# Kernel tuning notes

Measured on AMD Instinct MI355X. Metric: run time of the kernel, lower is better.

## Reference

```python
import jax, jax.numpy as jnp
import numpy as np

B, NQ, NK, D = 8, 2048, 2048, 256


def setup_inputs() -> dict:
    key = jax.random.key(0)
    ks = jax.random.split(key, 4)
    scale = 1.0 / np.sqrt(D)
    return {
        "query": jax.random.normal(ks[0], (B, NQ, D), dtype=jnp.float32),
        "key": jax.random.normal(ks[1], (B, NK, D), dtype=jnp.float32),
        "Wq": jax.random.normal(ks[2], (D, D), dtype=jnp.float32) * scale,
        "bq": jnp.zeros((D,), dtype=jnp.float32),
        "Wk": jax.random.normal(ks[3], (D, D), dtype=jnp.float32) * scale,
        "bk": jnp.zeros((D,), dtype=jnp.float32),
    }


def reference(query, key, Wq, bq, Wk, bk):
    # value = key (pre-projection), as in the torch module
    value = key
    # FFT over the sequence axis (dim=1), keep real part
    q = jnp.real(jnp.fft.fft(query, axis=1)).astype(query.dtype)
    # torch nn.Linear: y = x @ W.T + b
    q = q @ Wq.T + bq                      # [B, NQ, D]
    k = key @ Wk.T + bk                    # [B, NK, D]
    scale = 1.0 / jnp.sqrt(jnp.asarray(q.shape[-1], q.dtype))
    scores = jnp.einsum('bqd,bkd->bqk', q, k) * scale   # [B, NQ, NK]
    probs = jax.nn.softmax(scores, axis=-1)
    out = jnp.einsum('bqk,bkd->bqd', probs, value)       # [B, NQ, D]
    return out
```

## Files before the change

### kernel.cpp

```cpp
#include <hip/hip_runtime.h>

#define B_ 8
#define NQ_ 2048
#define NK_ 2048
#define D_ 256
#define KF_ 1056

typedef __attribute__((ext_vector_type(8))) short bf16x8_t;
typedef __attribute__((ext_vector_type(4))) float f32x4_t;

static __device__ __forceinline__ unsigned short f2bf(float x) {
  unsigned int u = __float_as_uint(x);
  unsigned int r = (u + 0x7FFFu + ((u >> 16) & 1u)) >> 16;
  return (unsigned short)r;
}
static __device__ __forceinline__ float bf2f(unsigned short b) {
  return __uint_as_float(((unsigned int)b) << 16);
}

typedef __attribute__((address_space(1))) unsigned int gas_u32;
typedef __attribute__((address_space(3))) unsigned int las_u32;
static __device__ __forceinline__ void gl16(const void* g, void* l) {
  __builtin_amdgcn_global_load_lds((const gas_u32*)g, (las_u32*)l, 16, 0, 0);
}

__global__ __launch_bounds__(256) void wsplit_kernel(const float* __restrict__ Wq,
                                                     const float* __restrict__ Wk,
                                                     unsigned short* __restrict__ Wqh,
                                                     unsigned short* __restrict__ Wql,
                                                     unsigned short* __restrict__ Wkh,
                                                     unsigned short* __restrict__ Wkl) {
  const int i = blockIdx.x * 256 + threadIdx.x;
  const int n = D_ * D_;
  const float* x = (i < n) ? Wq : Wk;
  unsigned short* xh = (i < n) ? Wqh : Wkh;
  unsigned short* xl = (i < n) ? Wql : Wkl;
  const int j = (i < n) ? i : i - n;
  const float v = x[j];
  const unsigned short hb = f2bf(v);
  xh[j] = hb;
  xl[j] = f2bf(v - bf2f(hb));
}

__global__ __launch_bounds__(256) void key_split_vt(const float* __restrict__ key,
                                                    unsigned short* __restrict__ keyh,
                                                    unsigned short* __restrict__ keyl,
                                                    unsigned short* __restrict__ Vt) {
  __shared__ unsigned short lds[32][258];
  const int t = threadIdx.x;
  const int j0 = blockIdx.x * 32;
  const int b  = blockIdx.y;
#pragma unroll
  for (int p = 0; p < 32; ++p) {
    const size_t g = ((size_t)b * NK_ + j0 + p) * D_ + t;
    const float v = key[g];
    const unsigned short hb = f2bf(v);
    keyh[g] = hb;
    keyl[g] = f2bf(v - bf2f(hb));
    lds[p][t] = hb;
  }
  __syncthreads();
#pragma unroll
  for (int p = 0; p < 32; ++p) {
    const int jj = t & 31;
    const int d  = (t >> 5) + 8 * p;
    Vt[((size_t)b * D_ + d) * NK_ + j0 + jj] = lds[jj][d];
  }
}

__global__ __launch_bounds__(256) void cos_split_kernel(unsigned short* __restrict__ Ch,
                                                        unsigned short* __restrict__ Cl) {
  const int idx = blockIdx.x * 256 + threadIdx.x;
  const int i = idx / KF_, n = idx % KF_;
  float c = 0.f;
  if (n <= 1024) {
    const int m = (i * n) & 2047;
    c = cosf((float)m * 0.0030679615757712823f);
  }
  const unsigned short hb = f2bf(c);
  Ch[idx] = hb;
  Cl[idx] = f2bf(c - bf2f(hb));
}

__global__ __launch_bounds__(256) void qtf_split_kernel(const float* __restrict__ q,
                                                        unsigned short* __restrict__ Qtfh,
                                                        unsigned short* __restrict__ Qtfl) {
  __shared__ float lds[32][33];
  const int t  = threadIdx.x;
  const int n0 = blockIdx.x * 32;
  const int d0 = blockIdx.y * 32;
  const int b  = blockIdx.z;
#pragma unroll
  for (int p = 0; p < 4; ++p) {
    const int idx = t + 256 * p;
    const int dd = idx & 31, nn = idx >> 5;
    const int n = n0 + nn;
    float v = 0.f;
    if (n <= 1024) v = q[((size_t)b * NQ_ + n) * D_ + d0 + dd];
    if (n >= 1 && n <= 1023) v += q[((size_t)b * NQ_ + (2048 - n)) * D_ + d0 + dd];
    lds[nn][dd] = v;
  }
  __syncthreads();
#pragma unroll
  for (int p = 0; p < 4; ++p) {
    const int idx = t + 256 * p;
    const int nn = idx & 31, dd = idx >> 5;
    const float v = lds[nn][dd];
    const unsigned short hb = f2bf(v);
    const size_t o = ((size_t)b * D_ + d0 + dd) * KF_ + n0 + nn;
    Qtfh[o] = hb;
    Qtfl[o] = f2bf(v - bf2f(hb));
  }
}

__global__ __launch_bounds__(256, 2) void dft_mfma(const unsigned short* __restrict__ Ch,
                                                   const unsigned short* __restrict__ Cl,
                                                   const unsigned short* __restrict__ Qtfh,
                                                   const unsigned short* __restrict__ Qtfl,
                                                   float* __restrict__ qr) {
  __shared__ __align__(16) unsigned short Ah[128][40];
  __shared__ __align__(16) unsigned short Al[128][40];
  __shared__ __align__(16) unsigned short Bh[128][40];
  __shared__ __align__(16) unsigned short Bl[128][40];
  const int t = threadIdx.x;
  const int b = blockIdx.z / 3, split = blockIdx.z % 3;
  const int i0 = blockIdx.x * 128, d0 = blockIdx.y * 128;
  const int w = t >> 6, lane = t & 63, quad = lane >> 4, l16 = lane & 15;
  const int wq = w & 1, wj = w >> 1;
  float* qrs = qr + (size_t)split * ((size_t)B_ * 1152 * D_);

  f32x4_t acc[4][4];
#pragma unroll
  for (int a = 0; a < 4; ++a)
#pragma unroll
    for (int c = 0; c < 4; ++c) acc[a][c] = (f32x4_t)0.f;

  const size_t abase = (size_t)i0 * KF_;
  const size_t bbase = ((size_t)b * D_ + d0) * KF_;

  for (int c0 = split * 352; c0 < split * 352 + 352; c0 += 32) {
#pragma unroll
    for (int it = 0; it < 2; ++it) {
      const int unit = t + 256 * it;
      const int row = unit >> 2, u = (unit & 3) * 8;
      const size_t go = (size_t)row * KF_ + c0 + u;
      *(uint4*)&Ah[row][u] = *(const uint4*)&Ch[abase + go];
      *(uint4*)&Al[row][u] = *(const uint4*)&Cl[abase + go];
      *(uint4*)&Bh[row][u] = *(const uint4*)&Qtfh[bbase + go];
      *(uint4*)&Bl[row][u] = *(const uint4*)&Qtfl[bbase + go];
    }
    __syncthreads();
    {
      const int dcol = quad * 8;
      bf16x8_t ah[4], al[4], bh[4], bl[4];
#pragma unroll
      for (int x = 0; x < 4; ++x) {
        ah[x] = *(const bf16x8_t*)&Ah[wq * 64 + x * 16 + l16][dcol];
        al[x] = *(const bf16x8_t*)&Al[wq * 64 + x * 16 + l16][dcol];
        bh[x] = *(const bf16x8_t*)&Bh[wj * 64 + x * 16 + l16][dcol];
        bl[x] = *(const bf16x8_t*)&Bl[wj * 64 + x * 16 + l16][dcol];
      }
#pragma unroll
      for (int at = 0; at < 4; ++at)
#pragma unroll
        for (int jt = 0; jt < 4; ++jt) {
          acc[at][jt] = __builtin_amdgcn_mfma_f32_16x16x32_bf16(ah[at], bh[jt], acc[at][jt], 0, 0, 0);
          acc[at][jt] = __builtin_amdgcn_mfma_f32_16x16x32_bf16(ah[at], bl[jt], acc[at][jt], 0, 0, 0);
          acc[at][jt] = __builtin_amdgcn_mfma_f32_16x16x32_bf16(al[at], bh[jt], acc[at][jt], 0, 0, 0);
        }
    }
    __syncthreads();
  }
#pragma unroll
  for (int at = 0; at < 4; ++at) {
#pragma unroll
    for (int jt = 0; jt < 4; ++jt) {
      const int d = d0 + wj * 64 + jt * 16 + l16;
#pragma unroll
      for (int r = 0; r < 4; ++r) {
        const int i = i0 + wq * 64 + at * 16 + quad * 4 + r;
        qrs[((size_t)b * 1152 + i) * D_ + d] = acc[at][jt][r];
      }
    }
  }
}

__global__ __launch_bounds__(256) void qr_finalize_kernel(const float* __restrict__ qr,
                                                          unsigned short* __restrict__ qrh,
                                                          unsigned short* __restrict__ qrl) {
  const int i = blockIdx.x, b = blockIdx.y, d = threadIdx.x;
  const int src = (i <= 1087) ? i : (2048 - i);
  const size_t S = (size_t)B_ * 1152 * D_;
  const size_t idx = ((size_t)b * 1152 + src) * D_ + d;
  const float v = qr[idx] + qr[idx + S] + qr[idx + 2 * S];
  const unsigned short hb = f2bf(v);
  const size_t o = ((size_t)b * NQ_ + i) * D_ + d;
  qrh[o] = hb;
  qrl[o] = f2bf(v - bf2f(hb));
}

__global__ __launch_bounds__(256, 2) void proj_mfma2(
    const unsigned short* __restrict__ xh0, const unsigned short* __restrict__ xl0,
    const unsigned short* __restrict__ Wh0, const unsigned short* __restrict__ Wl0,
    const float* __restrict__ b0,
    unsigned short* __restrict__ yh0, unsigned short* __restrict__ yl0,
    const unsigned short* __restrict__ xh1, const unsigned short* __restrict__ xl1,
    const unsigned short* __restrict__ Wh1, const unsigned short* __restrict__ Wl1,
    const float* __restrict__ b1,
    unsigned short* __restrict__ yh1, unsigned short* __restrict__ yl1) {
  const int z = blockIdx.z;
  const unsigned short* xh = z ? xh1 : xh0;
  const unsigned short* xl = z ? xl1 : xl0;
  const unsigned short* Wh = z ? Wh1 : Wh0;
  const unsigned short* Wl = z ? Wl1 : Wl0;
  const float* bias = z ? b1 : b0;
  unsigned short* yh = z ? yh1 : yh0;
  unsigned short* yl = z ? yl1 : yl0;

  __shared__ __align__(16) unsigned short Xh[128][72];
  __shared__ __align__(16) unsigned short Xl[128][72];
  __shared__ __align__(16) unsigned short Bh[128][72];
  __shared__ __align__(16) unsigned short Bl[128][72];
  const int t = threadIdx.x;
  const int m0 = blockIdx.x * 128, o0 = blockIdx.y * 128;
  const int w = t >> 6, lane = t & 63, quad = lane >> 4, l16 = lane & 15;
  const int wq = w & 1, wj = w >> 1;

  f32x4_t acc[4][4];
#pragma unroll
  for (int a = 0; a < 4; ++a)
#pragma unroll
    for (int c = 0; c < 4; ++c) acc[a][c] = (f32x4_t)0.f;

  const size_t xbase = (size_t)m0 * D_;
  const size_t wbase = (size_t)o0 * D_;

  for (int c0 = 0; c0 < D_; c0 += 64) {
#pragma unroll
    for (int it = 0; it < 4; ++it) {
      const int unit = t + 256 * it;
      const int row = unit >> 3, u = (unit & 7) * 8;
      const size_t go = (size_t)row * D_ + c0 + u;
      *(uint4*)&Xh[row][u] = *(const uint4*)&xh[xbase + go];
      *(uint4*)&Xl[row][u] = *(const uint4*)&xl[xbase + go];
      *(uint4*)&Bh[row][u] = *(const uint4*)&Wh[wbase + go];
      *(uint4*)&Bl[row][u] = *(const uint4*)&Wl[wbase + go];
    }
    __syncthreads();
#pragma unroll
    for (int ks = 0; ks < 2; ++ks) {
      const int dcol = ks * 32 + quad * 8;
      bf16x8_t ah[4], al[4], bh[4], bl[4];
#pragma unroll
      for (int x = 0; x < 4; ++x) {
        ah[x] = *(const bf16x8_t*)&Xh[wq * 64 + x * 16 + l16][dcol];
        al[x] = *(const bf16x8_t*)&Xl[wq * 64 + x * 16 + l16][dcol];
        bh[x] = *(const bf16x8_t*)&Bh[wj * 64 + x * 16 + l16][dcol];
        bl[x] = *(const bf16x8_t*)&Bl[wj * 64 + x * 16 + l16][dcol];
      }
#pragma unroll
      for (int at = 0; at < 4; ++at)
#pragma unroll
        for (int jt = 0; jt < 4; ++jt) {
          acc[at][jt] = __builtin_amdgcn_mfma_f32_16x16x32_bf16(ah[at], bh[jt], acc[at][jt], 0, 0, 0);
          acc[at][jt] = __builtin_amdgcn_mfma_f32_16x16x32_bf16(ah[at], bl[jt], acc[at][jt], 0, 0, 0);
          acc[at][jt] = __builtin_amdgcn_mfma_f32_16x16x32_bf16(al[at], bh[jt], acc[at][jt], 0, 0, 0);
        }
    }
    __syncthreads();
  }
#pragma unroll
  for (int at = 0; at < 4; ++at) {
#pragma unroll
    for (int jt = 0; jt < 4; ++jt) {
      const int o = o0 + wj * 64 + jt * 16 + l16;
      const float bv = bias[o];
#pragma unroll
      for (int r = 0; r < 4; ++r) {
        const int m = m0 + wq * 64 + at * 16 + quad * 4 + r;
        const float v = acc[at][jt][r] + bv;
        const unsigned short hb = f2bf(v);
        yh[(size_t)m * D_ + o] = hb;
        yl[(size_t)m * D_ + o] = f2bf(v - bf2f(hb));
      }
    }
  }
}

__global__ __launch_bounds__(512, 4) void scores_p(const unsigned short* __restrict__ qh,
                                                   const unsigned short* __restrict__ ql,
                                                   const unsigned short* __restrict__ kh,
                                                   const unsigned short* __restrict__ kl,
                                                   unsigned short* __restrict__ Pb,
                                                   float2* __restrict__ stat) {
  __shared__ __align__(16) unsigned short Qh[128][64];
  __shared__ __align__(16) unsigned short Ql[128][64];
  __shared__ __align__(16) unsigned short Kh[128][64];
  __shared__ __align__(16) unsigned short Kl[128][64];
  __shared__ float mred[2][128];
  __shared__ float lred[2][128];
  const int t = threadIdx.x;
  const int b = blockIdx.z;
  const int i0 = blockIdx.x * 128, j0 = blockIdx.y * 128;
  const int jb = blockIdx.y;
  const int w = t >> 6, lane = t & 63, quad = lane >> 4, l16 = lane & 15;
  const int wq = w & 3, wj = w >> 2;
  const int sr0 = t >> 3, ssl = t & 7;

  f32x4_t acc[2][4];
#pragma unroll
  for (int x = 0; x < 2; ++x)
#pragma unroll
    for (int y = 0; y < 4; ++y) acc[x][y] = (f32x4_t)0.f;

  const size_t qbase = ((size_t)b * NQ_ + i0) * D_;
  const size_t kbase = ((size_t)b * NK_ + j0) * D_;

  auto STAGE = [&](int c0) {
#pragma unroll
    for (int half = 0; half < 2; ++half) {
      const int row = half * 64 + sr0;
      const int sg = (ssl ^ (row & 7)) * 8;
      const size_t ro = (size_t)row * D_ + c0 + sg;
      gl16(qh + qbase + ro, &Qh[half * 64 + w * 8][0]);
      gl16(ql + qbase + ro, &Ql[half * 64 + w * 8][0]);
      gl16(kh + kbase + ro, &Kh[half * 64 + w * 8][0]);
      gl16(kl + kbase + ro, &Kl[half * 64 + w * 8][0]);
    }
  };

  STAGE(0);

#pragma unroll
  for (int s = 0; s < 4; ++s) {
    asm volatile("s_waitcnt vmcnt(0)" ::: "memory");
    __builtin_amdgcn_s_barrier();
    asm volatile("" ::: "memory");

#pragma unroll
    for (int ks = 0; ks < 2; ++ks) {
      bf16x8_t ah[2], al[2], bh[4], bl[4];
#pragma unroll
      for (int x = 0; x < 2; ++x) {
        const int ar = wq * 32 + x * 16 + l16;
        const int asl = ((ks * 4 + quad) ^ (ar & 7)) * 8;
        ah[x] = *(const bf16x8_t*)&Qh[ar][asl];
        al[x] = *(const bf16x8_t*)&Ql[ar][asl];
      }
#pragma unroll
      for (int y = 0; y < 4; ++y) {
        const int br = wj * 64 + y * 16 + l16;
        const int bsl = ((ks * 4 + quad) ^ (br & 7)) * 8;
        bh[y] = *(const bf16x8_t*)&Kh[br][bsl];
        bl[y] = *(const bf16x8_t*)&Kl[br][bsl];
      }
#pragma unroll
      for (int x = 0; x < 2; ++x)
#pragma unroll
        for (int y = 0; y < 4; ++y) {
          acc[x][y] = __builtin_amdgcn_mfma_f32_16x16x32_bf16(ah[x], bh[y], acc[x][y], 0, 0, 0);
          acc[x][y] = __builtin_amdgcn_mfma_f32_16x16x32_bf16(ah[x], bl[y], acc[x][y], 0, 0, 0);
          acc[x][y] = __builtin_amdgcn_mfma_f32_16x16x32_bf16(al[x], bh[y], acc[x][y], 0, 0, 0);
        }
    }

    asm volatile("" ::: "memory");
    __builtin_amdgcn_s_barrier();
    asm volatile("" ::: "memory");
    if (s < 3) STAGE((s + 1) * 64);
  }

  const float scale = 0.0625f;
  float mt[2][4];
#pragma unroll
  for (int x = 0; x < 2; ++x)
#pragma unroll
    for (int r = 0; r < 4; ++r) mt[x][r] = -3e38f;
#pragma unroll
  for (int x = 0; x < 2; ++x)
#pragma unroll
    for (int y = 0; y < 4; ++y)
#pragma unroll
      for (int r = 0; r < 4; ++r) {
        acc[x][y][r] *= scale;
        mt[x][r] = fmaxf(mt[x][r], acc[x][y][r]);
      }
#pragma unroll
  for (int off = 1; off < 16; off <<= 1)
#pragma unroll
    for (int x = 0; x < 2; ++x)
#pragma unroll
      for (int r = 0; r < 4; ++r) mt[x][r] = fmaxf(mt[x][r], __shfl_xor(mt[x][r], off));
  if (l16 == 0) {
#pragma unroll
    for (int x = 0; x < 2; ++x)
#pragma unroll
      for (int r = 0; r < 4; ++r)
        mred[wj][wq * 32 + x * 16 + quad * 4 + r] = mt[x][r];
  }
  __syncthreads();
  float nrow[2][4], mu[2][4], lt[2][4];
#pragma unroll
  for (int x = 0; x < 2; ++x)
#pragma unroll
    for (int r = 0; r < 4; ++r) {
      const int rr = wq * 32 + x * 16 + quad * 4 + r;
      const float m = fmaxf(mred[0][rr], mred[1][rr]);
      const float n = ceilf(m * 1.44269504f);
      nrow[x][r] = n;
      mu[x][r] = n * 0.69314718056f;
      lt[x][r] = 0.f;
    }
  const size_t pbase = ((size_t)(b * 16 + jb)) * NQ_ * 128;
#pragma unroll
  for (int x = 0; x < 2; ++x)
#pragma unroll
    for (int y = 0; y < 4; ++y) {
      const int jloc = wj * 64 + y * 16 + l16;
#pragma unroll
      for (int r = 0; r < 4; ++r) {
        const int i = i0 + wq * 32 + x * 16 + quad * 4 + r;
        float p = __expf(acc[x][y][r] - mu[x][r]);
        p = fmaxf(p, 8.673617e-19f);
        lt[x][r] += p;
        Pb[pbase + (size_t)i * 128 + jloc] = f2bf(p);
      }
    }
#pragma unroll
  for (int off = 1; off < 16; off <<= 1)
#pragma unroll
    for (int x = 0; x < 2; ++x)
#pragma unroll
      for (int r = 0; r < 4; ++r) lt[x][r] += __shfl_xor(lt[x][r], off);
  if (l16 == 0) {
#pragma unroll
    for (int x = 0; x < 2; ++x)
#pragma unroll
      for (int r = 0; r < 4; ++r)
        lred[wj][wq * 32 + x * 16 + quad * 4 + r] = lt[x][r];
  }
  __syncthreads();
  if (wj == 0 && l16 == 0) {
#pragma unroll
    for (int x = 0; x < 2; ++x)
#pragma unroll
      for (int r = 0; r < 4; ++r) {
        const int rr = wq * 32 + x * 16 + quad * 4 + r;
        stat[(size_t)jb * (B_ * NQ_) + (size_t)b * NQ_ + i0 + rr] =
            make_float2(nrow[x][r], lred[0][rr] + lred[1][rr]);
      }
  }
}

__global__ __launch_bounds__(256) void rowfin_kernel(const float2* __restrict__ stat,
                                                     float2* __restrict__ srow) {
  const int i = blockIdx.x * 256 + threadIdx.x;
  float2 st[16];
  float m = -3e38f;
#pragma unroll
  for (int jb = 0; jb < 16; ++jb) {
    st[jb] = stat[(size_t)jb * (B_ * NQ_) + i];
    m = fmaxf(m, st[jb].x);
  }
  float l = 0.f;
#pragma unroll
  for (int jb = 0; jb < 16; ++jb) l += st[jb].y * exp2f(st[jb].x - m);
  srow[i] = make_float2(m, 1.0f / l);
}

__global__ __launch_bounds__(512, 1) void pv_p(const unsigned short* __restrict__ Pb,
                                               const float2* __restrict__ stat,
                                               const float2* __restrict__ srow,
                                               const unsigned short* __restrict__ Vt,
                                               float* __restrict__ out) {
  __shared__ __align__(16) unsigned short Ps[3][64][64];
  __shared__ __align__(16) unsigned short Vs[3][256][64];
  const int t = threadIdx.x;
  const int lb = (blockIdx.x & 7) * 32 + (blockIdx.x >> 3);
  const int mb = lb * 64;
  const int b  = lb >> 5;
  const int i0 = mb & (NQ_ - 1);
  const int w = t >> 6, lane = t & 63, quad = lane >> 4, l16 = lane & 15;
  const int wm = w & 1, wd = w >> 1;
  const int prow = t >> 3, pslot = t & 7;

  unsigned int es2[16][2];
  {
    float nmax[2];
#pragma unroll
    for (int x = 0; x < 2; ++x)
      nmax[x] = srow[mb + wm * 32 + x * 16 + l16].x;
#pragma unroll
    for (int jb = 0; jb < 16; ++jb)
#pragma unroll
      for (int x = 0; x < 2; ++x) {
        const int arow = mb + wm * 32 + x * 16 + l16;
        int e = (int)(nmax[x] - stat[(size_t)jb * (B_ * NQ_) + arow].x);
        e = e < 0 ? 0 : (e > 60 ? 60 : e);
        es2[jb][x] = (unsigned int)(e << 7) * 0x00010001u;
      }
  }

  f32x4_t acc[2][4];
#pragma unroll
  for (int x = 0; x < 2; ++x)
#pragma unroll
    for (int y = 0; y < 4; ++y) acc[x][y] = (f32x4_t)0.f;

  const size_t vbase = (size_t)b * D_ * (size_t)NK_;

  auto STAGE = [&](int nb, int s) {
    const int jj = s * 64;
    const int jb = jj >> 7, off = jj & 127;
    {
      const int sg = pslot ^ (prow & 7);
      gl16(Pb + ((size_t)(b * 16 + jb)) * NQ_ * 128 +
               (size_t)(i0 + prow) * 128 + off + sg * 8,
           &Ps[nb][w * 8][0]);
    }
#pragma unroll
    for (int k = 0; k < 4; ++k) {
      const int vrow = k * 64 + prow;
      const int sg = pslot ^ (vrow & 7);
      gl16(Vt + vbase + (size_t)vrow * NK_ + jj + sg * 8,
           &Vs[nb][k * 64 + w * 8][0]);
    }
  };

  asm volatile("s_waitcnt vmcnt(0)" ::: "memory");
  STAGE(0, 0);
  STAGE(1, 1);

#pragma unroll
  for (int s = 0; s < 32; ++s) {
    const int cb = s % 3;
    if (s < 30) {
      STAGE((s + 2) % 3, s + 2);
      asm volatile("s_waitcnt vmcnt(10)" ::: "memory");
    } else if (s == 30) {
      asm volatile("s_waitcnt vmcnt(5)" ::: "memory");
    } else {
      asm volatile("s_waitcnt vmcnt(0)" ::: "memory");
    }
    __builtin_amdgcn_s_barrier();
    asm volatile("" ::: "memory");

    const unsigned int e0 = es2[s >> 1][0], e1 = es2[s >> 1][1];
#pragma unroll
    for (int ks = 0; ks < 2; ++ks) {
      bf16x8_t a[2], bv[4];
#pragma unroll
      for (int x = 0; x < 2; ++x) {
        const int row = wm * 32 + x * 16 + l16;
        const int sk = (ks * 4 + quad) ^ (row & 7);
        uint4 u = *(const uint4*)&Ps[cb][row][sk * 8];
        const unsigned int e = (x == 0) ? e0 : e1;
        u.x -= e; u.y -= e; u.z -= e; u.w -= e;
        a[x] = *(const bf16x8_t*)&u;
      }
#pragma unroll
      for (int y = 0; y < 4; ++y) {
        const int row = wd * 64 + y * 16 + l16;
        const int sk = (ks * 4 + quad) ^ (row & 7);
        bv[y] = *(const bf16x8_t*)&Vs[cb][row][sk * 8];
      }
#pragma unroll
      for (int x = 0; x < 2; ++x)
#pragma unroll
        for (int y = 0; y < 4; ++y)
          acc[x][y] = __builtin_amdgcn_mfma_f32_16x16x32_bf16(a[x], bv[y], acc[x][y], 0, 0, 0);
    }

    asm volatile("" ::: "memory");
    __builtin_amdgcn_s_barrier();
    asm volatile("" ::: "memory");
  }

#pragma unroll
  for (int x = 0; x < 2; ++x) {
    float sy[4];
#pragma unroll
    for (int r = 0; r < 4; ++r)
      sy[r] = srow[mb + wm * 32 + x * 16 + quad * 4 + r].y;
#pragma unroll
    for (int y = 0; y < 4; ++y) {
      const int d = wd * 64 + y * 16 + l16;
#pragma unroll
      for (int r = 0; r < 4; ++r) {
        const int m = mb + wm * 32 + x * 16 + quad * 4 + r;
        out[(size_t)m * D_ + d] = acc[x][y][r] * sy[r];
      }
    }
  }
}

extern "C" void kernel_launch(void* const* d_in, const int* in_sizes, int n_in,
                              void* d_out, int out_size, void* d_ws, size_t ws_size,
                              hipStream_t stream) {
  const float* query = (const float*)d_in[0];
  const float* key   = (const float*)d_in[1];
  const float* Wq    = (const float*)d_in[2];
  const float* bq    = (const float*)d_in[3];
  const float* Wk    = (const float*)d_in[4];
  const float* bk    = (const float*)d_in[5];
  float* out = (float*)d_out;

  char* ws = (char*)d_ws;
  const size_t MB = (size_t)1 << 20;
  unsigned short* qh = (unsigned short*)(ws);
  unsigned short* ql = (unsigned short*)(ws + 8 * MB);
  unsigned short* kh = (unsigned short*)(ws + 16 * MB);
  unsigned short* kl = (unsigned short*)(ws + 24 * MB);
  unsigned short* Vt = (unsigned short*)(ws + 32 * MB);
  unsigned short* Pb = (unsigned short*)(ws + 40 * MB);
  float2* stat = (float2*)(ws + 108 * MB);
  float2* srow = (float2*)(ws + 110 * MB);
  unsigned short* Ch   = (unsigned short*)(ws + 40 * MB);
  unsigned short* Cl   = (unsigned short*)(ws + 43 * MB);
  unsigned short* Qtfh = (unsigned short*)(ws + 46 * MB);
  unsigned short* Qtfl = (unsigned short*)(ws + 51 * MB);
  float*          qr   = (float*)(ws + 56 * MB);
  unsigned short* qrh  = (unsigned short*)(ws + 40 * MB);
  unsigned short* qrl  = (unsigned short*)(ws + 48 * MB);
  unsigned short* keyh = (unsigned short*)(ws + 92 * MB);
  unsigned short* keyl = (unsigned short*)(ws + 100 * MB);
  unsigned short* Wqh  = (unsigned short*)(ws + 111 * MB);
  unsigned short* Wql  = (unsigned short*)(ws + 111 * MB + 256 * 1024);
  unsigned short* Wkh  = (unsigned short*)(ws + 111 * MB + 512 * 1024);
  unsigned short* Wkl  = (unsigned short*)(ws + 111 * MB + 768 * 1024);

  dim3 blk(256);

  key_split_vt<<<dim3(NK_ / 32, B_), blk, 0, stream>>>(key, keyh, keyl, Vt);
  wsplit_kernel<<<2 * D_ * D_ / 256, blk, 0, stream>>>(Wq, Wk, Wqh, Wql, Wkh, Wkl);
  cos_split_kernel<<<1152 * KF_ / 256, blk, 0, stream>>>(Ch, Cl);
  qtf_split_kernel<<<dim3(KF_ / 32, D_ / 32, B_), blk, 0, stream>>>(query, Qtfh, Qtfl);
  dft_mfma<<<dim3(9, 2, B_ * 3), blk, 0, stream>>>(Ch, Cl, Qtfh, Qtfl, qr);
  qr_finalize_kernel<<<dim3(2048, B_), blk, 0, stream>>>(qr, qrh, qrl);
  proj_mfma2<<<dim3(B_ * NQ_ / 128, 2, 2), blk, 0, stream>>>(
      qrh, qrl, Wqh, Wql, bq, qh, ql,
      keyh, keyl, Wkh, Wkl, bk, kh, kl);
  scores_p<<<dim3(NQ_ / 128, NK_ / 128, B_), dim3(512), 0, stream>>>(qh, ql, kh, kl, Pb, stat);
  rowfin_kernel<<<B_ * NQ_ / 256, blk, 0, stream>>>(stat, srow);
  pv_p<<<dim3(256), dim3(512), 0, stream>>>(Pb, stat, srow, Vt, out);
}
```

Before: 192.4 us.

## Merge prep kernels into one launch and fold row finalize into PV

Four small preprocessing kernels (key split/transpose, weight split, cosine table, query fold) are combined into a single kernel that dispatches on block index. The row-statistics finalize kernel is removed: each PV block now reduces the per-tile max and sum for its own rows and gets the inverse sum to the output lanes with a wave shuffle. This cuts four kernel launches and a small global round trip, at the cost of some redundant stat reads in PV and the larger shared-memory size of the merged prep kernel.

```diff
diff --git a/kernel.cpp b/kernel.cpp
--- a/kernel.cpp
+++ b/kernel.cpp
@@ -24,92 +24,95 @@
   __builtin_amdgcn_global_load_lds((const gas_u32*)g, (las_u32*)l, 16, 0, 0);
 }
 
-__global__ __launch_bounds__(256) void wsplit_kernel(const float* __restrict__ Wq,
-                                                     const float* __restrict__ Wk,
-                                                     unsigned short* __restrict__ Wqh,
-                                                     unsigned short* __restrict__ Wql,
-                                                     unsigned short* __restrict__ Wkh,
-                                                     unsigned short* __restrict__ Wkl) {
-  const int i = blockIdx.x * 256 + threadIdx.x;
-  const int n = D_ * D_;
-  const float* x = (i < n) ? Wq : Wk;
-  unsigned short* xh = (i < n) ? Wqh : Wkh;
-  unsigned short* xl = (i < n) ? Wql : Wkl;
-  const int j = (i < n) ? i : i - n;
-  const float v = x[j];
-  const unsigned short hb = f2bf(v);
-  xh[j] = hb;
-  xl[j] = f2bf(v - bf2f(hb));
-}
-
-__global__ __launch_bounds__(256) void key_split_vt(const float* __restrict__ key,
-                                                    unsigned short* __restrict__ keyh,
-                                                    unsigned short* __restrict__ keyl,
-                                                    unsigned short* __restrict__ Vt) {
-  __shared__ unsigned short lds[32][258];
+__global__ __launch_bounds__(256) void prep_all(const float* __restrict__ key,
+                                                unsigned short* __restrict__ keyh,
+                                                unsigned short* __restrict__ keyl,
+                                                unsigned short* __restrict__ Vt,
+                                                const float* __restrict__ Wq,
+                                                const float* __restrict__ Wk,
+                                                unsigned short* __restrict__ Wqh,
+                                                unsigned short* __restrict__ Wql,
+                                                unsigned short* __restrict__ Wkh,
+                                                unsigned short* __restrict__ Wkl,
+                                                unsigned short* __restrict__ Ch,
+                                                unsigned short* __restrict__ Cl,
+                                                const float* __restrict__ q,
+                                                unsigned short* __restrict__ Qtfh,
+                                                unsigned short* __restrict__ Qtfl) {
+  __shared__ __align__(16) char smem[16512];
+  const int bid = blockIdx.x;
   const int t = threadIdx.x;
-  const int j0 = blockIdx.x * 32;
-  const int b  = blockIdx.y;
-#pragma unroll
-  for (int p = 0; p < 32; ++p) {
-    const size_t g = ((size_t)b * NK_ + j0 + p) * D_ + t;
-    const float v = key[g];
+
+  if (bid < 512) {
+    unsigned short (*lds)[258] = (unsigned short (*)[258])smem;
+    const int j0 = (bid & 63) * 32;
+    const int b  = bid >> 6;
+#pragma unroll
+    for (int p = 0; p < 32; ++p) {
+      const size_t g = ((size_t)b * NK_ + j0 + p) * D_ + t;
+      const float v = key[g];
+      const unsigned short hb = f2bf(v);
+      keyh[g] = hb;
+      keyl[g] = f2bf(v - bf2f(hb));
+      lds[p][t] = hb;
+    }
+    __syncthreads();
+#pragma unroll
+    for (int p = 0; p < 32; ++p) {
+      const int jj = t & 31;
+      const int d  = (t >> 5) + 8 * p;
+      Vt[((size_t)b * D_ + d) * NK_ + j0 + jj] = lds[jj][d];
+    }
+  } else if (bid < 1024) {
+    const int i = (bid - 512) * 256 + t;
+    const int n = D_ * D_;
+    const float* x = (i < n) ? Wq : Wk;
+    unsigned short* xh = (i < n) ? Wqh : Wkh;
+    unsigned short* xl = (i < n) ? Wql : Wkl;
+    const int j = (i < n) ? i : i - n;
+    const float v = x[j];
     const unsigned short hb = f2bf(v);
-    keyh[g] = hb;
-    keyl[g] = f2bf(v - bf2f(hb));
-    lds[p][t] = hb;
-  }
-  __syncthreads();
-#pragma unroll
-  for (int p = 0; p < 32; ++p) {
-    const int jj = t & 31;
-    const int d  = (t >> 5) + 8 * p;
-    Vt[((size_t)b * D_ + d) * NK_ + j0 + jj] = lds[jj][d];
-  }
-}
-
-__global__ __launch_bounds__(256) void cos_split_kernel(unsigned short* __restrict__ Ch,
-                                                        unsigned short* __restrict__ Cl) {
-  const int idx = blockIdx.x * 256 + threadIdx.x;
-  const int i = idx / KF_, n = idx % KF_;
-  float c = 0.f;
-  if (n <= 1024) {
-    const int m = (i * n) & 2047;
-    c = cosf((float)m * 0.0030679615757712823f);
-  }
-  const unsigned short hb = f2bf(c);
-  Ch[idx] = hb;
-  Cl[idx] = f2bf(c - bf2f(hb));
-}
-
-__global__ __launch_bounds__(256) void qtf_split_kernel(const float* __restrict__ q,
-                                                        unsigned short* __restrict__ Qtfh,
-                                                        unsigned short* __restrict__ Qtfl) {
-  __shared__ float lds[32][33];
-  const int t  = threadIdx.x;
-  const int n0 = blockIdx.x * 32;
-  const int d0 = blockIdx.y * 32;
-  const int b  = blockIdx.z;
-#pragma unroll
-  for (int p = 0; p < 4; ++p) {
-    const int idx = t + 256 * p;
-    const int dd = idx & 31, nn = idx >> 5;
-    const int n = n0 + nn;
-    float v = 0.f;
-    if (n <= 1024) v = q[((size_t)b * NQ_ + n) * D_ + d0 + dd];
-    if (n >= 1 && n <= 1023) v += q[((size_t)b * NQ_ + (2048 - n)) * D_ + d0 + dd];
-    lds[nn][dd] = v;
-  }
-  __syncthreads();
-#pragma unroll
-  for (int p = 0; p < 4; ++p) {
-    const int idx = t + 256 * p;
-    const int nn = idx & 31, dd = idx >> 5;
-    const float v = lds[nn][dd];
-    const unsigned short hb = f2bf(v);
-    const size_t o = ((size_t)b * D_ + d0 + dd) * KF_ + n0 + nn;
-    Qtfh[o] = hb;
-    Qtfl[o] = f2bf(v - bf2f(hb));
+    xh[j] = hb;
+    xl[j] = f2bf(v - bf2f(hb));
+  } else if (bid < 5776) {
+    const int idx = (bid - 1024) * 256 + t;
+    const int i = idx / KF_, n = idx % KF_;
+    float c = 0.f;
+    if (n <= 1024) {
+      const int m = (i * n) & 2047;
+      c = cosf((float)m * 0.0030679615757712823f);
+    }
+    const unsigned short hb = f2bf(c);
+    Ch[idx] = hb;
+    Cl[idx] = f2bf(c - bf2f(hb));
+  } else {
+    float (*lds)[33] = (float (*)[33])smem;
+    const int vb = bid - 5776;
+    const int n0 = (vb % 33) * 32;
+    const int rest = vb / 33;
+    const int d0 = (rest & 7) * 32;
+    const int b  = rest >> 3;
+#pragma unroll
+    for (int p = 0; p < 4; ++p) {
+      const int idx = t + 256 * p;
+      const int dd = idx & 31, nn = idx >> 5;
+      const int n = n0 + nn;
+      float v = 0.f;
+      if (n <= 1024) v = q[((size_t)b * NQ_ + n) * D_ + d0 + dd];
+      if (n >= 1 && n <= 1023) v += q[((size_t)b * NQ_ + (2048 - n)) * D_ + d0 + dd];
+      lds[nn][dd] = v;
+    }
+    __syncthreads();
+#pragma unroll
+    for (int p = 0; p < 4; ++p) {
+      const int idx = t + 256 * p;
+      const int nn = idx & 31, dd = idx >> 5;
+      const float v = lds[nn][dd];
+      const unsigned short hb = f2bf(v);
+      const size_t o = ((size_t)b * D_ + d0 + dd) * KF_ + n0 + nn;
+      Qtfh[o] = hb;
+      Qtfl[o] = f2bf(v - bf2f(hb));
+    }
   }
 }
 
@@ -452,25 +455,8 @@
   }
 }
 
-__global__ __launch_bounds__(256) void rowfin_kernel(const float2* __restrict__ stat,
-                                                     float2* __restrict__ srow) {
-  const int i = blockIdx.x * 256 + threadIdx.x;
-  float2 st[16];
-  float m = -3e38f;
-#pragma unroll
-  for (int jb = 0; jb < 16; ++jb) {
-    st[jb] = stat[(size_t)jb * (B_ * NQ_) + i];
-    m = fmaxf(m, st[jb].x);
-  }
-  float l = 0.f;
-#pragma unroll
-  for (int jb = 0; jb < 16; ++jb) l += st[jb].y * exp2f(st[jb].x - m);
-  srow[i] = make_float2(m, 1.0f / l);
-}
-
 __global__ __launch_bounds__(512, 1) void pv_p(const unsigned short* __restrict__ Pb,
                                                const float2* __restrict__ stat,
-                                               const float2* __restrict__ srow,
                                                const unsigned short* __restrict__ Vt,
                                                float* __restrict__ out) {
   __shared__ __align__(16) unsigned short Ps[3][64][64];
@@ -485,20 +471,26 @@
   const int prow = t >> 3, pslot = t & 7;
 
   unsigned int es2[16][2];
-  {
-    float nmax[2];
-#pragma unroll
-    for (int x = 0; x < 2; ++x)
-      nmax[x] = srow[mb + wm * 32 + x * 16 + l16].x;
-#pragma unroll
-    for (int jb = 0; jb < 16; ++jb)
-#pragma unroll
-      for (int x = 0; x < 2; ++x) {
-        const int arow = mb + wm * 32 + x * 16 + l16;
-        int e = (int)(nmax[x] - stat[(size_t)jb * (B_ * NQ_) + arow].x);
-        e = e < 0 ? 0 : (e > 60 ? 60 : e);
-        es2[jb][x] = (unsigned int)(e << 7) * 0x00010001u;
-      }
+  float linv[2];
+#pragma unroll
+  for (int x = 0; x < 2; ++x) {
+    const int arow = mb + wm * 32 + x * 16 + l16;
+    float2 st[16];
+    float m = -3e38f;
+#pragma unroll
+    for (int jb = 0; jb < 16; ++jb) {
+      st[jb] = stat[(size_t)jb * (B_ * NQ_) + arow];
+      m = fmaxf(m, st[jb].x);
+    }
+    float l = 0.f;
+#pragma unroll
+    for (int jb = 0; jb < 16; ++jb) {
+      l += st[jb].y * exp2f(st[jb].x - m);
+      int e = (int)(m - st[jb].x);
+      e = e < 0 ? 0 : (e > 60 ? 60 : e);
+      es2[jb][x] = (unsigned int)(e << 7) * 0x00010001u;
+    }
+    linv[x] = 1.0f / l;
   }
 
   f32x4_t acc[2][4];
@@ -581,7 +573,7 @@
     float sy[4];
 #pragma unroll
     for (int r = 0; r < 4; ++r)
-      sy[r] = srow[mb + wm * 32 + x * 16 + quad * 4 + r].y;
+      sy[r] = __shfl(linv[x], quad * 4 + r);
 #pragma unroll
     for (int y = 0; y < 4; ++y) {
       const int d = wd * 64 + y * 16 + l16;
@@ -614,7 +606,6 @@
   unsigned short* Vt = (unsigned short*)(ws + 32 * MB);
   unsigned short* Pb = (unsigned short*)(ws + 40 * MB);
   float2* stat = (float2*)(ws + 108 * MB);
-  float2* srow = (float2*)(ws + 110 * MB);
   unsigned short* Ch   = (unsigned short*)(ws + 40 * MB);
   unsigned short* Cl   = (unsigned short*)(ws + 43 * MB);
   unsigned short* Qtfh = (unsigned short*)(ws + 46 * MB);
@@ -631,16 +622,14 @@
 
   dim3 blk(256);
 
-  key_split_vt<<<dim3(NK_ / 32, B_), blk, 0, stream>>>(key, keyh, keyl, Vt);
-  wsplit_kernel<<<2 * D_ * D_ / 256, blk, 0, stream>>>(Wq, Wk, Wqh, Wql, Wkh, Wkl);
-  cos_split_kernel<<<1152 * KF_ / 256, blk, 0, stream>>>(Ch, Cl);
-  qtf_split_kernel<<<dim3(KF_ / 32, D_ / 32, B_), blk, 0, stream>>>(query, Qtfh, Qtfl);
+  prep_all<<<7888, blk, 0, stream>>>(key, keyh, keyl, Vt, Wq, Wk,
+                                     Wqh, Wql, Wkh, Wkl, Ch, Cl,
+                                     query, Qtfh, Qtfl);
   dft_mfma<<<dim3(9, 2, B_ * 3), blk, 0, stream>>>(Ch, Cl, Qtfh, Qtfl, qr);
   qr_finalize_kernel<<<dim3(2048, B_), blk, 0, stream>>>(qr, qrh, qrl);
   proj_mfma2<<<dim3(B_ * NQ_ / 128, 2, 2), blk, 0, stream>>>(
       qrh, qrl, Wqh, Wql, bq, qh, ql,
       keyh, keyl, Wkh, Wkl, bk, kh, kl);
   scores_p<<<dim3(NQ_ / 128, NK_ / 128, B_), dim3(512), 0, stream>>>(qh, ql, kh, kl, Pb, stat);
-  rowfin_kernel<<<B_ * NQ_ / 256, blk, 0, stream>>>(stat, srow);
-  pv_p<<<dim3(256), dim3(512), 0, stream>>>(Pb, stat, srow, Vt, out);
-}
+  pv_p<<<dim3(256), dim3(512), 0, stream>>>(Pb, stat, Vt, out);
+}
```

Measured after the change: 184.3 us, median of 2. 4.2% less time.
